# Kernel optimization log

Hardware: AMD Instinct MI355X
Metric: run time of the kernel (lower is better)

## Reference

```python
import jax, jax.numpy as jnp
import numpy as np

DIM = 192
HEADS = 4
CTX = 256
HID = int(DIM * 2.66)  # 510


def _dwconv(x, w):
    # x: (b,c,h,w), w: (c,1,3,3) depthwise
    return jax.lax.conv_general_dilated(
        x, w, window_strides=(1, 1), padding='SAME',
        dimension_numbers=('NCHW', 'OIHW', 'NCHW'),
        feature_group_count=x.shape[1])


def _conv1x1(x, w):
    # w: (out, in)
    return jnp.einsum('oc,bchw->bohw', w, x)


def _layernorm(x, weight, bias):
    # WithBias LayerNorm over channel dim (last dim after to_3d == channels)
    mu = x.mean(axis=1, keepdims=True)
    var = ((x - mu) ** 2).mean(axis=1, keepdims=True)
    xn = (x - mu) / jnp.sqrt(var + 1e-5)
    return xn * weight[None, :, None, None] + bias[None, :, None, None]


def setup_inputs() -> dict:
    key = jax.random.key(0)
    ks = jax.random.split(key, 16)
    s = 0.02
    inp = {
        'x': jax.random.normal(ks[0], (8, DIM, 128, 128), jnp.float32),
        'context_emb': jax.random.normal(ks[1], (8, CTX), jnp.float32),
        'ln1_w': jnp.ones((DIM,), jnp.float32),
        'ln1_b': jnp.zeros((DIM,), jnp.float32),
        'ln2_w': jnp.ones((DIM,), jnp.float32),
        'ln2_b': jnp.zeros((DIM,), jnp.float32),
        'w_qkv': jax.random.normal(ks[2], (3 * DIM, DIM), jnp.float32) * s,
        'w_qkv_dw': jax.random.normal(ks[3], (3 * DIM, 1, 3, 3), jnp.float32) * s,
        'w_proj': jax.random.normal(ks[4], (DIM, DIM), jnp.float32) * s,
        'base_temp': jnp.ones((HEADS, 1, 1), jnp.float32),
        'ta_w1': jax.random.normal(ks[5], (DIM // 4, CTX), jnp.float32) * s,
        'ta_b1': jnp.zeros((DIM // 4,), jnp.float32),
        'ta_w2': jax.random.normal(ks[6], (HEADS, DIM // 4), jnp.float32) * s,
        'ta_b2': jnp.zeros((HEADS,), jnp.float32),
        'vg_w': jax.random.normal(ks[7], (DIM, CTX), jnp.float32) * s,
        'vg_b': jnp.zeros((DIM,), jnp.float32),
        'w_local': jax.random.normal(ks[8], (DIM, 1, 3, 3), jnp.float32) * s,
        'w_ffn_in': jax.random.normal(ks[9], (2 * HID, DIM), jnp.float32) * s,
        'w_ffn_dw': jax.random.normal(ks[10], (2 * HID, 1, 3, 3), jnp.float32) * s,
        'w_ffn_out': jax.random.normal(ks[11], (DIM, HID), jnp.float32) * s,
    }
    return inp


def _forward(x, context_emb, ln1_w, ln1_b, ln2_w, ln2_b, w_qkv, w_qkv_dw,
             w_proj, base_temp, ta_w1, ta_b1, ta_w2, ta_b2, vg_w, vg_b,
             w_local, w_ffn_in, w_ffn_dw, w_ffn_out):
    b, c, h, w = x.shape
    hd = c // HEADS
    scale = hd ** (-0.5)

    # ---- Attention branch ----
    residual = x
    xn = _layernorm(x, ln1_w, ln1_b)

    # context adapters
    t = jax.nn.relu(context_emb @ ta_w1.T + ta_b1) @ ta_w2.T + ta_b2  # (b,heads)
    temp_factor = jax.nn.sigmoid(t)[:, :, None, None] * 2.0 + 0.5    # (b,heads,1,1)
    total_temp = base_temp[None] * temp_factor
    v_gate = jax.nn.sigmoid(context_emb @ vg_w.T + vg_b)             # (b,dim)
    v_gate = v_gate.reshape(b, HEADS, hd, 1)

    qkv = _dwconv(_conv1x1(xn, w_qkv), w_qkv_dw)
    q, k, v = jnp.split(qkv, 3, axis=1)

    def heads_flat(t4):
        return t4.reshape(b, HEADS, hd, h * w)

    qf = heads_flat(q)
    kf = heads_flat(k)
    vf = heads_flat(v)
    qf = qf / jnp.maximum(jnp.linalg.norm(qf, axis=-1, keepdims=True), 1e-12)
    kf = kf / jnp.maximum(jnp.linalg.norm(kf, axis=-1, keepdims=True), 1e-12)

    attn = jnp.einsum('bhcn,bhdn->bhcd', qf, kf) * scale  # (b,heads,hd,hd)
    attn = jax.nn.softmax(attn * total_temp, axis=-1)

    out_global = jnp.einsum('bhcd,bhdn->bhcn', attn, vf * v_gate)
    out_global = out_global.reshape(b, c, h, w)
    out_local = _dwconv(v, w_local)
    x = residual + _conv1x1(out_global + out_local, w_proj)

    # ---- GDFN branch ----
    residual = x
    xn = _layernorm(x, ln2_w, ln2_b)
    y = _dwconv(_conv1x1(xn, w_ffn_in), w_ffn_dw)
    y1, y2 = jnp.split(y, 2, axis=1)
    y = jax.nn.gelu(y1, approximate=False) * y2
    x = residual + _conv1x1(y, w_ffn_out)
    return x


def reference(x, context_emb, ln1_w, ln1_b, ln2_w, ln2_b, w_qkv, w_qkv_dw,
              w_proj, base_temp, ta_w1, ta_b1, ta_w2, ta_b2, vg_w, vg_b,
              w_local, w_ffn_in, w_ffn_dw, w_ffn_out):
    return _forward(x, context_emb, ln1_w, ln1_b, ln2_w, ln2_b, w_qkv,
                    w_qkv_dw, w_proj, base_temp, ta_w1, ta_b1, ta_w2, ta_b2,
                    vg_w, vg_b, w_local, w_ffn_in, w_ffn_dw, w_ffn_out)
```

## Files before the change

kernel.cpp:

```cpp
#include <hip/hip_runtime.h>
#include <math.h>

#define NB 8
#define NC 192
#define NH 128
#define NW 128
#define HW 16384
#define NQ 576
#define NHID 510
#define NHIDP 512
#define NG2 1020
#define NG2P 1024

#define BROWS 32
#define BSLOTS 34
#define BPIX (BSLOTS * NW)
#define BIPIX (BROWS * NW)

typedef unsigned short u16;
typedef short s16x8 __attribute__((ext_vector_type(8)));
typedef float f32x4 __attribute__((ext_vector_type(4)));

#define MFMA_BF16(a, b, c) __builtin_amdgcn_mfma_f32_16x16x32_bf16((a), (b), (c), 0, 0, 0)

__device__ __forceinline__ u16 f2bf(float f) {
  union { float f; unsigned u; } v; v.f = f;
  unsigned r = v.u + 0x7fffu + ((v.u >> 16) & 1u);
  return (u16)(r >> 16);
}
__device__ __forceinline__ float bf2f(u16 h) {
  union { unsigned u; float f; } v; v.u = ((unsigned)h) << 16; return v.f;
}
__device__ __forceinline__ float lo2f(unsigned u) {
  union { unsigned u; float f; } v; v.u = u << 16; return v.f;
}
__device__ __forceinline__ float hi2f(unsigned u) {
  union { unsigned u; float f; } v; v.u = u & 0xffff0000u; return v.f;
}

__global__ void k_prep(const float* __restrict__ wq, const float* __restrict__ wfi,
                       const float* __restrict__ wfo,
                       u16* __restrict__ oq, u16* __restrict__ ofi, u16* __restrict__ ofo) {
  const int n1 = NQ * NC, n2 = NG2P * NC, n3 = NC * NHIDP;
  for (int i = blockIdx.x * blockDim.x + threadIdx.x; i < n1 + n2 + n3;
       i += gridDim.x * blockDim.x) {
    if (i < n1) {
      oq[i] = f2bf(wq[i]);
    } else if (i < n1 + n2) {
      int j = i - n1; int row = j / NC;
      u16 v = 0;
      if (row < NG2) v = f2bf(wfi[j]);
      ofi[j] = v;
    } else {
      int j = i - n1 - n2; int row = j >> 9, col = j & 511;
      u16 v = 0;
      if (col < NHID) v = f2bf(wfo[row * NHID + col]);
      ofo[j] = v;
    }
  }
}

__global__ void k_ctx(const float* __restrict__ ce, const float* __restrict__ taw1,
                      const float* __restrict__ tab1, const float* __restrict__ taw2,
                      const float* __restrict__ tab2, const float* __restrict__ vgw,
                      const float* __restrict__ vgb, const float* __restrict__ btemp,
                      float* __restrict__ tempt, float* __restrict__ vg) {
  int b = blockIdx.x, t = threadIdx.x;
  __shared__ float sce[256];
  __shared__ float shid[48];
  sce[t] = ce[b * 256 + t];
  __syncthreads();
  if (t < 48) {
    float s = tab1[t];
    for (int j = 0; j < 256; j++) s = fmaf(taw1[t * 256 + j], sce[j], s);
    shid[t] = fmaxf(s, 0.f);
  }
  __syncthreads();
  if (t < 4) {
    float s = tab2[t];
    for (int j = 0; j < 48; j++) s = fmaf(taw2[t * 48 + j], shid[j], s);
    float sg = 1.f / (1.f + expf(-s));
    tempt[b * 4 + t] = btemp[t] * (sg * 2.f + 0.5f);
  }
  if (t < 192) {
    float s = vgb[t];
    for (int j = 0; j < 256; j++) s = fmaf(vgw[t * 256 + j], sce[j], s);
    vg[b * 192 + t] = 1.f / (1.f + expf(-s));
  }
}

__global__ __launch_bounds__(256, 2)
void k_ln_gemm_band(const float* __restrict__ in, const float* __restrict__ lnw,
                    const float* __restrict__ lnb, const u16* __restrict__ wbf,
                    u16* __restrict__ out, int nchunks, int row_start, int slot0) {
  __shared__ u16 Xn[64 * 200];
  __shared__ u16 Wc[64 * 200];
  __shared__ float red[512];
  __shared__ float stats[128];
  int t = threadIdx.x;
  int lane = t & 63, wv = t >> 6;
  int bpb = gridDim.x >> 3;
  int b = blockIdx.x / bpb;
  int rb = blockIdx.x - b * bpb;
  int gpx0 = row_start * NW + rb * 64;
  int opx0 = slot0 * NW + rb * 64;
  const float* xp = in + (size_t)b * NC * HW + gpx0 + lane;
  float vals[48];
  float s = 0.f, s2 = 0.f;
#pragma unroll
  for (int j = 0; j < 48; j++) {
    float v = xp[(size_t)(wv * 48 + j) * HW];
    vals[j] = v; s += v; s2 = fmaf(v, v, s2);
  }
  red[wv * 64 + lane] = s;
  red[256 + wv * 64 + lane] = s2;
  __syncthreads();
  if (t < 64) {
    float m = 0.f, q = 0.f;
#pragma unroll
    for (int k = 0; k < 4; k++) { m += red[k * 64 + t]; q += red[256 + k * 64 + t]; }
    m *= (1.f / 192.f);
    float var = q * (1.f / 192.f) - m * m;
    stats[t] = m; stats[64 + t] = rsqrtf(var + 1e-5f);
  }
  __syncthreads();
  float mu = stats[lane], rs = stats[64 + lane];
#pragma unroll
  for (int j = 0; j < 48; j += 2) {
    int c = wv * 48 + j;
    float xa = (vals[j] - mu) * rs * lnw[c] + lnb[c];
    float xb = (vals[j + 1] - mu) * rs * lnw[c + 1] + lnb[c + 1];
    *(unsigned*)&Xn[lane * 200 + c] = (unsigned)f2bf(xa) | ((unsigned)f2bf(xb) << 16);
  }
  int r = lane & 15, grp = lane >> 4;
  int ostride = nchunks << 6;
  for (int nc = 0; nc < nchunks; nc++) {
    __syncthreads();
    for (int i = t; i < 1536; i += 256) {
      int row = i / 24, sg = i % 24;
      *(s16x8*)&Wc[row * 200 + sg * 8] =
          *(const s16x8*)&wbf[(size_t)(nc * 64 + row) * 192 + sg * 8];
    }
    __syncthreads();
    f32x4 z = {0.f, 0.f, 0.f, 0.f};
    f32x4 acc0 = z, acc1 = z, acc2 = z, acc3 = z;
#pragma unroll
    for (int ks = 0; ks < 6; ks++) {
      int k0 = ks * 32 + grp * 8;
      s16x8 a = *(s16x8*)&Xn[(wv * 16 + r) * 200 + k0];
      acc0 = MFMA_BF16(a, *(s16x8*)&Wc[r * 200 + k0], acc0);
      acc1 = MFMA_BF16(a, *(s16x8*)&Wc[(16 + r) * 200 + k0], acc1);
      acc2 = MFMA_BF16(a, *(s16x8*)&Wc[(32 + r) * 200 + k0], acc2);
      acc3 = MFMA_BF16(a, *(s16x8*)&Wc[(48 + r) * 200 + k0], acc3);
    }
    u16* op = out + ((size_t)b * BPIX + opx0 + wv * 16 + grp * 4) * ostride + nc * 64 + r;
#pragma unroll
    for (int i = 0; i < 4; i++) {
      op[(size_t)i * ostride] = f2bf(acc0[i]);
      op[(size_t)i * ostride + 16] = f2bf(acc1[i]);
      op[(size_t)i * ostride + 32] = f2bf(acc2[i]);
      op[(size_t)i * ostride + 48] = f2bf(acc3[i]);
    }
  }
}

__global__ __launch_bounds__(256, 4)
void k_dw_attn_band(const u16* __restrict__ qb_band, const float* __restrict__ wdw,
                    u16* __restrict__ qkb, u16* __restrict__ vpm,
                    float* __restrict__ ssq, int r0) {
  __shared__ u16 Hl[6 * 18 * 64];
  __shared__ float sred[8 * 64];
  int t = threadIdx.x;
  int cc = blockIdx.x % 9;
  int rem = blockIdx.x / 9;
  int b = rem >> 6; int r2 = rem & 63;
  int h0l = (r2 >> 3) * 4, w0 = (r2 & 7) * 16;
  int c0 = cc * 64;
  const s16x8 z8 = {0, 0, 0, 0, 0, 0, 0, 0};
  for (int i = t; i < 864; i += 256) {
    int px = i >> 3, sg = i & 7;
    int hh = px / 18, ww = px % 18;
    int slot = h0l + hh;
    int gh = r0 - 1 + slot;
    int gw = w0 - 1 + ww;
    s16x8 v = z8;
    if (gh >= 0 && gh < NH && gw >= 0 && gw < NW)
      v = *(const s16x8*)&qb_band[((size_t)b * BPIX + slot * NW + gw) * NQ + c0 + sg * 8];
    *(s16x8*)&Hl[(hh * 18 + ww) * 64 + sg * 8] = v;
  }
  __syncthreads();
  int cp = t & 31, psub = t >> 5;
  int pr = psub >> 1, pc0 = (psub & 1) * 8;
  int gc = c0 + 2 * cp;
  float wg0[9], wg1[9];
#pragma unroll
  for (int q = 0; q < 9; q++) { wg0[q] = wdw[gc * 9 + q]; wg1[q] = wdw[(gc + 1) * 9 + q]; }
  bool isv = (c0 >= 384);
  float sq0 = 0.f, sq1 = 0.f;
  s16x8 ov0 = z8, ov1 = z8;
#pragma unroll
  for (int j = 0; j < 8; j++) {
    int pc = pc0 + j;
    float a0 = 0.f, a1 = 0.f;
#pragma unroll
    for (int dr = 0; dr < 3; dr++)
#pragma unroll
      for (int dc = 0; dc < 3; dc++) {
        unsigned u = *(const unsigned*)&Hl[((pr + dr) * 18 + pc + dc) * 64 + 2 * cp];
        a0 = fmaf(lo2f(u), wg0[dr * 3 + dc], a0);
        a1 = fmaf(hi2f(u), wg1[dr * 3 + dc], a1);
      }
    u16 u0 = f2bf(a0), u1 = f2bf(a1);
    if (isv) {
      int gp = (r0 + h0l + pr) * NW + w0 + pc;
      *(unsigned*)&vpm[((size_t)b * HW + gp) * 192 + (gc - 384)] =
          (unsigned)u0 | ((unsigned)u1 << 16);
    } else {
      ov0[j] = (short)u0; ov1[j] = (short)u1;
      float f0 = bf2f(u0), f1 = bf2f(u1);
      sq0 = fmaf(f0, f0, sq0); sq1 = fmaf(f1, f1, sq1);
    }
  }
  if (!isv) {
    int lpx = (h0l + pr) * NW + w0 + pc0;
    *(s16x8*)&qkb[((size_t)b * 384 + gc) * BIPIX + lpx] = ov0;
    *(s16x8*)&qkb[((size_t)b * 384 + gc + 1) * BIPIX + lpx] = ov1;
    sred[psub * 64 + 2 * cp] = sq0;
    sred[psub * 64 + 2 * cp + 1] = sq1;
    __syncthreads();
    if (t < 64) {
      float sa = 0.f;
#pragma unroll
      for (int p8 = 0; p8 < 8; p8++) sa += sred[p8 * 64 + t];
      atomicAdd(&ssq[b * 384 + c0 + t], sa);
    }
  }
}

__global__ __launch_bounds__(256, 2)
void k_attn_band(const u16* __restrict__ qkb, float* __restrict__ attn) {
  __shared__ float par[4 * 2304];
  int t = threadIdx.x;
  int lane = t & 63, wv = t >> 6;
  int r = lane & 15, grp = lane >> 4;
  int bh = blockIdx.x >> 2, kc = blockIdx.x & 3;
  int b = bh >> 2, h = bh & 3;
  const u16* qb = qkb + ((size_t)b * 384 + h * 48) * BIPIX;
  const u16* kb = qkb + ((size_t)b * 384 + 192 + h * 48) * BIPIX;
  f32x4 z = {0.f, 0.f, 0.f, 0.f};
  f32x4 acc[3][3];
#pragma unroll
  for (int i = 0; i < 3; i++)
#pragma unroll
    for (int j = 0; j < 3; j++) acc[i][j] = z;
  int kbase = kc * 1024 + wv * 256 + grp * 8;
#pragma unroll 2
  for (int ks = 0; ks < 8; ks++) {
    int k0 = kbase + ks * 32;
    s16x8 af[3], bf[3];
#pragma unroll
    for (int mt = 0; mt < 3; mt++) af[mt] = *(const s16x8*)&qb[(size_t)(mt * 16 + r) * BIPIX + k0];
#pragma unroll
    for (int nt = 0; nt < 3; nt++) bf[nt] = *(const s16x8*)&kb[(size_t)(nt * 16 + r) * BIPIX + k0];
#pragma unroll
    for (int mt = 0; mt < 3; mt++)
#pragma unroll
      for (int nt = 0; nt < 3; nt++) acc[mt][nt] = MFMA_BF16(af[mt], bf[nt], acc[mt][nt]);
  }
#pragma unroll
  for (int mt = 0; mt < 3; mt++)
#pragma unroll
    for (int nt = 0; nt < 3; nt++)
#pragma unroll
      for (int i = 0; i < 4; i++)
        par[wv * 2304 + (mt * 16 + grp * 4 + i) * 48 + nt * 16 + r] = acc[mt][nt][i];
  __syncthreads();
  float* ag = attn + (size_t)bh * 2304;
  for (int i = t; i < 2304; i += 256)
    atomicAdd(&ag[i], par[i] + par[2304 + i] + par[4608 + i] + par[6912 + i]);
}

__global__ void k_softmax(float* __restrict__ attn, const float* __restrict__ ssq,
                          const float* __restrict__ tempt, const float* __restrict__ vg) {
  int bh = blockIdx.x, b = bh >> 2, h = bh & 3;
  int t = threadIdx.x;
  __shared__ float srk[48], svg[48];
  if (t < 48) {
    float nk = sqrtf(ssq[b * 384 + 192 + h * 48 + t]);
    srk[t] = 1.f / fmaxf(nk, 1e-12f);
    svg[t] = vg[b * 192 + h * 48 + t];
  }
  __syncthreads();
  if (t < 48) {
    float nq = sqrtf(ssq[b * 384 + h * 48 + t]);
    float rq = 1.f / fmaxf(nq, 1e-12f);
    float sc = 0.14433756729740643f * tempt[b * 4 + h] * rq;
    float* row = attn + (size_t)bh * 2304 + t * 48;
    float l[48]; float mx = -1e30f;
#pragma unroll
    for (int d = 0; d < 48; d++) { l[d] = row[d] * srk[d] * sc; mx = fmaxf(mx, l[d]); }
    float ss = 0.f;
#pragma unroll
    for (int d = 0; d < 48; d++) { l[d] = expf(l[d] - mx); ss += l[d]; }
    float inv = 1.f / ss;
#pragma unroll
    for (int d = 0; d < 48; d++) row[d] = l[d] * inv * svg[d];
  }
}

__global__ __launch_bounds__(256)
void k_wd(const float* __restrict__ attn, const float* __restrict__ wp,
          u16* __restrict__ wdg) {
  __shared__ float am[4 * 48 * 48];
  int b = blockIdx.x >> 3, oc = blockIdx.x & 7;
  int t = threadIdx.x;
  const float* ag = attn + (size_t)b * 4 * 2304;
  for (int i = t; i < 9216; i += 256) am[i] = ag[i];
  __syncthreads();
  u16* wdb = wdg + (size_t)b * 192 * 384;
  for (int idx = t; idx < 24 * 384; idx += 256) {
    int oo = idx / 384, j = idx % 384;
    int o = oc * 24 + oo;
    float val;
    if (j < 192) {
      int hj = j / 48, dj = j % 48;
      const float* wpo = wp + o * 192 + hj * 48;
      const float* ap = am + hj * 2304 + dj;
      float sa = 0.f;
#pragma unroll
      for (int c = 0; c < 48; c++) sa = fmaf(wpo[c], ap[c * 48], sa);
      val = sa;
    } else {
      val = wp[o * 192 + (j - 192)];
    }
    wdb[o * 384 + j] = f2bf(val);
  }
}

__global__ __launch_bounds__(256, 2)
void k_proj(const u16* __restrict__ vpm, const float* __restrict__ wl,
            const u16* __restrict__ wdg, const float* __restrict__ x,
            float* __restrict__ x2) {
  __shared__ u16 Hl[6 * 18 * 64];
  __shared__ u16 Xl[64 * 392];
  int t = threadIdx.x;
  int b = blockIdx.x >> 8; int r2 = blockIdx.x & 255;
  int h0 = (r2 >> 3) * 4, w0 = (r2 & 7) * 16;
  int cp = t & 31, psub = t >> 5;
  int pr = psub >> 1, pc0 = (psub & 1) * 8;
  int lane = t & 63, wv = t >> 6;
  int r = lane & 15, grp = lane >> 4;
  float xres[3][4][4];
#pragma unroll
  for (int mt = 0; mt < 3; mt++)
#pragma unroll
    for (int nt = 0; nt < 4; nt++) {
      size_t base = ((size_t)b * NC + wv * 48 + mt * 16 + grp * 4) * HW +
                    (h0 + nt) * NW + w0 + r;
#pragma unroll
      for (int i = 0; i < 4; i++) xres[mt][nt][i] = x[base + (size_t)i * HW];
    }
  const s16x8 z8 = {0, 0, 0, 0, 0, 0, 0, 0};
  for (int c3 = 0; c3 < 3; c3++) {
    int c0 = c3 * 64;
    __syncthreads();
    for (int i = t; i < 864; i += 256) {
      int px = i >> 3, sg = i & 7;
      int hh = px / 18, ww = px % 18;
      int gh = h0 - 1 + hh, gw = w0 - 1 + ww;
      s16x8 v = z8;
      if (gh >= 0 && gh < NH && gw >= 0 && gw < NW)
        v = *(const s16x8*)&vpm[((size_t)b * HW + gh * NW + gw) * 192 + c0 + sg * 8];
      *(s16x8*)&Hl[(hh * 18 + ww) * 64 + sg * 8] = v;
    }
    __syncthreads();
    int gc = c0 + 2 * cp;
    float wg0[9], wg1[9];
#pragma unroll
    for (int q = 0; q < 9; q++) { wg0[q] = wl[gc * 9 + q]; wg1[q] = wl[(gc + 1) * 9 + q]; }
#pragma unroll
    for (int j = 0; j < 8; j++) {
      int pc = pc0 + j; int p = pr * 16 + pc;
      float a0 = 0.f, a1 = 0.f; unsigned uc = 0;
#pragma unroll
      for (int dr = 0; dr < 3; dr++)
#pragma unroll
        for (int dc = 0; dc < 3; dc++) {
          unsigned u = *(const unsigned*)&Hl[((pr + dr) * 18 + pc + dc) * 64 + 2 * cp];
          if (dr == 1 && dc == 1) uc = u;
          a0 = fmaf(lo2f(u), wg0[dr * 3 + dc], a0);
          a1 = fmaf(hi2f(u), wg1[dr * 3 + dc], a1);
        }
      *(unsigned*)&Xl[p * 392 + gc] = uc;
      *(unsigned*)&Xl[p * 392 + 192 + gc] =
          (unsigned)f2bf(a0) | ((unsigned)f2bf(a1) << 16);
    }
  }
  __syncthreads();
  const u16* wdb = wdg + (size_t)b * 192 * 384;
  f32x4 z = {0.f, 0.f, 0.f, 0.f};
  f32x4 acc[3][4];
#pragma unroll
  for (int i = 0; i < 3; i++)
#pragma unroll
    for (int j = 0; j < 4; j++) acc[i][j] = z;
#pragma unroll 2
  for (int ks = 0; ks < 12; ks++) {
    int k0 = ks * 32 + grp * 8;
    s16x8 b0 = *(s16x8*)&Xl[r * 392 + k0];
    s16x8 b1 = *(s16x8*)&Xl[(16 + r) * 392 + k0];
    s16x8 b2 = *(s16x8*)&Xl[(32 + r) * 392 + k0];
    s16x8 b3 = *(s16x8*)&Xl[(48 + r) * 392 + k0];
#pragma unroll
    for (int mt = 0; mt < 3; mt++) {
      s16x8 a = *(const s16x8*)&wdb[(size_t)(wv * 48 + mt * 16 + r) * 384 + k0];
      acc[mt][0] = MFMA_BF16(a, b0, acc[mt][0]);
      acc[mt][1] = MFMA_BF16(a, b1, acc[mt][1]);
      acc[mt][2] = MFMA_BF16(a, b2, acc[mt][2]);
      acc[mt][3] = MFMA_BF16(a, b3, acc[mt][3]);
    }
  }
#pragma unroll
  for (int mt = 0; mt < 3; mt++)
#pragma unroll
    for (int nt = 0; nt < 4; nt++) {
      size_t base = ((size_t)b * NC + wv * 48 + mt * 16 + grp * 4) * HW +
                    (h0 + nt) * NW + w0 + r;
#pragma unroll
      for (int i = 0; i < 4; i++) {
        size_t idx = base + (size_t)i * HW;
        x2[idx] = acc[mt][nt][i] + xres[mt][nt][i];
      }
    }
}

__global__ __launch_bounds__(256, 2)
void k_gelu_ffn_band(const u16* __restrict__ ypre, const float* __restrict__ wdwf,
                     const u16* __restrict__ wfo, const float* __restrict__ x2,
                     float* __restrict__ out, int r0) {
  __shared__ u16 H1[6 * 18 * 64];
  __shared__ u16 H2[6 * 18 * 72];
  __shared__ u16 Yc[64 * 80];
  int t = threadIdx.x;
  int b = blockIdx.x >> 6; int r2 = blockIdx.x & 63;
  int h0l = (r2 >> 3) * 4, w0 = (r2 & 7) * 16;
  int cp = t & 31, psub = t >> 5;
  int pr = psub >> 1, pc0 = (psub & 1) * 8;
  int lane = t & 63, wv = t >> 6;
  int r = lane & 15, grp = lane >> 4;
  int jl = 2 * cp;
  float x2res[3][4][4];
#pragma unroll
  for (int mt = 0; mt < 3; mt++)
#pragma unroll
    for (int nt = 0; nt < 4; nt++) {
      size_t base = ((size_t)b * NC + wv * 48 + mt * 16 + grp * 4) * HW +
                    (r0 + h0l + nt) * NW + w0 + r;
#pragma unroll
      for (int i = 0; i < 4; i++) x2res[mt][nt][i] = x2[base + (size_t)i * HW];
    }
  const s16x8 z8 = {0, 0, 0, 0, 0, 0, 0, 0};
  f32x4 z = {0.f, 0.f, 0.f, 0.f};
  f32x4 acc[3][4];
#pragma unroll
  for (int i = 0; i < 3; i++)
#pragma unroll
    for (int j = 0; j < 4; j++) acc[i][j] = z;

  for (int jc = 0; jc < 8; jc++) {
    int j0 = jc * 64;
    int base2 = j0 + 504;
    __syncthreads();
    for (int i = t; i < 864; i += 256) {
      int px = i >> 3, sg = i & 7;
      int hh = px / 18, ww = px % 18;
      int slot = h0l + hh;
      int gh = r0 - 1 + slot, gw = w0 - 1 + ww;
      s16x8 v = z8;
      if (gh >= 0 && gh < NH && gw >= 0 && gw < NW)
        v = *(const s16x8*)&ypre[((size_t)b * BPIX + slot * NW + gw) * NG2P + j0 + sg * 8];
      *(s16x8*)&H1[(hh * 18 + ww) * 64 + sg * 8] = v;
    }
    for (int i = t; i < 972; i += 256) {
      int px = i / 9, sg = i % 9;
      int hh = px / 18, ww = px % 18;
      int slot = h0l + hh;
      int gh = r0 - 1 + slot, gw = w0 - 1 + ww;
      s16x8 v = z8;
      if (gh >= 0 && gh < NH && gw >= 0 && gw < NW)
        v = *(const s16x8*)&ypre[((size_t)b * BPIX + slot * NW + gw) * NG2P + base2 + sg * 8];
      *(s16x8*)&H2[(hh * 18 + ww) * 72 + sg * 8] = v;
    }
    __syncthreads();
    int j = j0 + jl;
    bool v0 = (j < NHID), v1 = (j + 1 < NHID);
    float w1a[9], w1b[9], w2a[9], w2b[9];
#pragma unroll
    for (int q = 0; q < 9; q++) {
      w1a[q] = 0.f; w1b[q] = 0.f; w2a[q] = 0.f; w2b[q] = 0.f;
      if (v0) { w1a[q] = wdwf[j * 9 + q]; w2a[q] = wdwf[(j + NHID) * 9 + q]; }
      if (v1) { w1b[q] = wdwf[(j + 1) * 9 + q]; w2b[q] = wdwf[(j + 1 + NHID) * 9 + q]; }
    }
#pragma unroll
    for (int jj = 0; jj < 8; jj++) {
      int pc = pc0 + jj;
      float d1a = 0.f, d1b = 0.f, d2a = 0.f, d2b = 0.f;
#pragma unroll
      for (int dr = 0; dr < 3; dr++)
#pragma unroll
        for (int dc = 0; dc < 3; dc++) {
          int q = dr * 3 + dc;
          unsigned u1 = *(const unsigned*)&H1[((pr + dr) * 18 + pc + dc) * 64 + jl];
          unsigned u2 = *(const unsigned*)&H2[((pr + dr) * 18 + pc + dc) * 72 + jl + 6];
          d1a = fmaf(lo2f(u1), w1a[q], d1a); d1b = fmaf(hi2f(u1), w1b[q], d1b);
          d2a = fmaf(lo2f(u2), w2a[q], d2a); d2b = fmaf(hi2f(u2), w2b[q], d2b);
        }
      float ga = 0.5f * d1a * (1.f + erff(d1a * 0.70710678118654752f));
      float gb = 0.5f * d1b * (1.f + erff(d1b * 0.70710678118654752f));
      float ya = v0 ? ga * d2a : 0.f;
      float yb = v1 ? gb * d2b : 0.f;
      int lp = pr * 16 + pc;
      *(unsigned*)&Yc[lp * 80 + jl] = (unsigned)f2bf(ya) | ((unsigned)f2bf(yb) << 16);
    }
    __syncthreads();
#pragma unroll
    for (int ks = 0; ks < 2; ks++) {
      int k0 = ks * 32 + grp * 8;
      s16x8 b0 = *(s16x8*)&Yc[r * 80 + k0];
      s16x8 b1 = *(s16x8*)&Yc[(16 + r) * 80 + k0];
      s16x8 b2 = *(s16x8*)&Yc[(32 + r) * 80 + k0];
      s16x8 b3 = *(s16x8*)&Yc[(48 + r) * 80 + k0];
#pragma unroll
      for (int mt = 0; mt < 3; mt++) {
        s16x8 a = *(const s16x8*)&wfo[(size_t)(wv * 48 + mt * 16 + r) * NHIDP + j0 + k0];
        acc[mt][0] = MFMA_BF16(a, b0, acc[mt][0]);
        acc[mt][1] = MFMA_BF16(a, b1, acc[mt][1]);
        acc[mt][2] = MFMA_BF16(a, b2, acc[mt][2]);
        acc[mt][3] = MFMA_BF16(a, b3, acc[mt][3]);
      }
    }
  }
#pragma unroll
  for (int mt = 0; mt < 3; mt++)
#pragma unroll
    for (int nt = 0; nt < 4; nt++) {
      size_t base = ((size_t)b * NC + wv * 48 + mt * 16 + grp * 4) * HW +
                    (r0 + h0l + nt) * NW + w0 + r;
#pragma unroll
      for (int i = 0; i < 4; i++) {
        size_t idx = base + (size_t)i * HW;
        out[idx] = acc[mt][nt][i] + x2res[mt][nt][i];
      }
    }
}

extern "C" void kernel_launch(void* const* d_in, const int* in_sizes, int n_in,
                              void* d_out, int out_size, void* d_ws, size_t ws_size,
                              hipStream_t stream) {
  const float* x      = (const float*)d_in[0];
  const float* ce     = (const float*)d_in[1];
  const float* ln1w   = (const float*)d_in[2];
  const float* ln1b   = (const float*)d_in[3];
  const float* ln2w   = (const float*)d_in[4];
  const float* ln2b   = (const float*)d_in[5];
  const float* wqkv   = (const float*)d_in[6];
  const float* wqkvdw = (const float*)d_in[7];
  const float* wproj  = (const float*)d_in[8];
  const float* btemp  = (const float*)d_in[9];
  const float* taw1   = (const float*)d_in[10];
  const float* tab1   = (const float*)d_in[11];
  const float* taw2   = (const float*)d_in[12];
  const float* tab2   = (const float*)d_in[13];
  const float* vgw    = (const float*)d_in[14];
  const float* vgb    = (const float*)d_in[15];
  const float* wlocal = (const float*)d_in[16];
  const float* wffni  = (const float*)d_in[17];
  const float* wffndw = (const float*)d_in[18];
  const float* wffno  = (const float*)d_in[19];
  float* outp = (float*)d_out;
  char* ws = (char*)d_ws;

  const size_t REQUIRED = 224602240ULL;
  if (ws_size < REQUIRED) {
    hipMemsetAsync(d_out, 0, (size_t)out_size * 4, stream);
    return;
  }
  u16*   wq_bf   = (u16*)(ws + 0);
  u16*   wfi_bf  = (u16*)(ws + 221184);
  u16*   wfo_bf  = (u16*)(ws + 614400);
  float* tempt   = (float*)(ws + 811008);
  float* vg      = (float*)(ws + 811136);
  float* ssq     = (float*)(ws + 817280);
  float* attn    = (float*)(ws + 829568);
  u16*   wdg     = (u16*)(ws + 1124480);
  u16*   qkvband = (u16*)(ws + 2304128);
  u16*   qkband  = (u16*)(ws + 42412160);
  u16*   ypreband= (u16*)(ws + 2304128);
  u16*   vpm     = (u16*)(ws + 73607296);
  float* x2      = (float*)(ws + 123938944);

  hipMemsetAsync(ws + 817280, 0, 12288 + 294912, stream);
  k_prep<<<512, 256, 0, stream>>>(wqkv, wffni, wffno, wq_bf, wfi_bf, wfo_bf);
  k_ctx<<<8, 256, 0, stream>>>(ce, taw1, tab1, taw2, tab2, vgw, vgb, btemp, tempt, vg);

  for (int band = 0; band < 4; band++) {
    int r0 = band * BROWS;
    int rs = (r0 > 0) ? r0 - 1 : 0;
    int re = (r0 + BROWS + 1 < NH) ? r0 + BROWS + 1 : NH;
    int nr = re - rs;
    int s0 = rs - (r0 - 1);
    k_ln_gemm_band<<<8 * nr * 2, 256, 0, stream>>>(x, ln1w, ln1b, wq_bf, qkvband, 9, rs, s0);
    k_dw_attn_band<<<9 * 8 * 64, 256, 0, stream>>>(qkvband, wqkvdw, qkband, vpm, ssq, r0);
    k_attn_band<<<32 * 4, 256, 0, stream>>>(qkband, attn);
  }
  k_softmax<<<32, 64, 0, stream>>>(attn, ssq, tempt, vg);
  k_wd<<<64, 256, 0, stream>>>(attn, wproj, wdg);
  k_proj<<<2048, 256, 0, stream>>>(vpm, wlocal, wdg, x, x2);

  for (int band = 0; band < 4; band++) {
    int r0 = band * BROWS;
    int rs = (r0 > 0) ? r0 - 1 : 0;
    int re = (r0 + BROWS + 1 < NH) ? r0 + BROWS + 1 : NH;
    int nr = re - rs;
    int s0 = rs - (r0 - 1);
    k_ln_gemm_band<<<8 * nr * 2, 256, 0, stream>>>(x2, ln2w, ln2b, wfi_bf, ypreband, 16, rs, s0);
    k_gelu_ffn_band<<<8 * 64, 256, 0, stream>>>(ypreband, wffndw, wfo_bf, x2, outp, r0);
  }
}
```

Before: 1.268 ms.

## Double-buffer halo tiles via direct global-to-LDS loads in depthwise kernels

Halo tile staging in the depthwise-conv kernels now uses direct global-to-LDS 16-byte loads, with out-of-bounds pixels pointing at a zeroed scratch buffer instead of taking a register path. k_proj and k_gelu_ffn_band double-buffer these tiles so the next channel chunk is fetched while the current one is computed, removing one barrier per iteration. The FFN kernel also stops holding residual values in registers and reads them at the epilogue, to ease register pressure. Doubling the LDS buffers may reduce occupancy.

Result: faster. 1.114 ms (-12.2%).

```diff
diff --git a/kernel.cpp b/kernel.cpp
--- a/kernel.cpp
+++ b/kernel.cpp
@@ -36,6 +36,12 @@
 }
 __device__ __forceinline__ float hi2f(unsigned u) {
   union { unsigned u; float f; } v; v.u = u & 0xffff0000u; return v.f;
+}
+
+__device__ __forceinline__ void gll16(const void* g, void* l) {
+  __builtin_amdgcn_global_load_lds(
+      (const __attribute__((address_space(1))) void*)g,
+      (__attribute__((address_space(3))) void*)l, 16, 0, 0);
 }
 
 __global__ void k_prep(const float* __restrict__ wq, const float* __restrict__ wfi,
@@ -167,7 +173,7 @@
 __global__ __launch_bounds__(256, 4)
 void k_dw_attn_band(const u16* __restrict__ qb_band, const float* __restrict__ wdw,
                     u16* __restrict__ qkb, u16* __restrict__ vpm,
-                    float* __restrict__ ssq, int r0) {
+                    float* __restrict__ ssq, int r0, const u16* __restrict__ zp) {
   __shared__ u16 Hl[6 * 18 * 64];
   __shared__ float sred[8 * 64];
   int t = threadIdx.x;
@@ -183,10 +189,10 @@
     int slot = h0l + hh;
     int gh = r0 - 1 + slot;
     int gw = w0 - 1 + ww;
-    s16x8 v = z8;
-    if (gh >= 0 && gh < NH && gw >= 0 && gw < NW)
-      v = *(const s16x8*)&qb_band[((size_t)b * BPIX + slot * NW + gw) * NQ + c0 + sg * 8];
-    *(s16x8*)&Hl[(hh * 18 + ww) * 64 + sg * 8] = v;
+    const void* g = (gh >= 0 && gh < NH && gw >= 0 && gw < NW)
+        ? (const void*)&qb_band[((size_t)b * BPIX + slot * NW + gw) * NQ + c0 + sg * 8]
+        : (const void*)zp;
+    gll16(g, &Hl[i * 8]);
   }
   __syncthreads();
   int cp = t & 31, psub = t >> 5;
@@ -340,8 +346,8 @@
 __global__ __launch_bounds__(256, 2)
 void k_proj(const u16* __restrict__ vpm, const float* __restrict__ wl,
             const u16* __restrict__ wdg, const float* __restrict__ x,
-            float* __restrict__ x2) {
-  __shared__ u16 Hl[6 * 18 * 64];
+            float* __restrict__ x2, const u16* __restrict__ zp) {
+  __shared__ u16 Hl[2][6 * 18 * 64];
   __shared__ u16 Xl[64 * 392];
   int t = threadIdx.x;
   int b = blockIdx.x >> 8; int r2 = blockIdx.x & 255;
@@ -360,20 +366,26 @@
 #pragma unroll
       for (int i = 0; i < 4; i++) xres[mt][nt][i] = x[base + (size_t)i * HW];
     }
-  const s16x8 z8 = {0, 0, 0, 0, 0, 0, 0, 0};
-  for (int c3 = 0; c3 < 3; c3++) {
-    int c0 = c3 * 64;
-    __syncthreads();
+
+  auto stageH = [&](int c3s, int buf) {
+    int c0s = c3s * 64;
     for (int i = t; i < 864; i += 256) {
       int px = i >> 3, sg = i & 7;
       int hh = px / 18, ww = px % 18;
       int gh = h0 - 1 + hh, gw = w0 - 1 + ww;
-      s16x8 v = z8;
-      if (gh >= 0 && gh < NH && gw >= 0 && gw < NW)
-        v = *(const s16x8*)&vpm[((size_t)b * HW + gh * NW + gw) * 192 + c0 + sg * 8];
-      *(s16x8*)&Hl[(hh * 18 + ww) * 64 + sg * 8] = v;
-    }
-    __syncthreads();
+      const void* g = (gh >= 0 && gh < NH && gw >= 0 && gw < NW)
+          ? (const void*)&vpm[((size_t)b * HW + gh * NW + gw) * 192 + c0s + sg * 8]
+          : (const void*)zp;
+      gll16(g, &Hl[buf][i * 8]);
+    }
+  };
+
+  stageH(0, 0);
+  __syncthreads();
+  int cur = 0;
+  for (int c3 = 0; c3 < 3; c3++) {
+    if (c3 < 2) stageH(c3 + 1, cur ^ 1);
+    int c0 = c3 * 64;
     int gc = c0 + 2 * cp;
     float wg0[9], wg1[9];
 #pragma unroll
@@ -386,7 +398,7 @@
       for (int dr = 0; dr < 3; dr++)
 #pragma unroll
         for (int dc = 0; dc < 3; dc++) {
-          unsigned u = *(const unsigned*)&Hl[((pr + dr) * 18 + pc + dc) * 64 + 2 * cp];
+          unsigned u = *(const unsigned*)&Hl[cur][((pr + dr) * 18 + pc + dc) * 64 + 2 * cp];
           if (dr == 1 && dc == 1) uc = u;
           a0 = fmaf(lo2f(u), wg0[dr * 3 + dc], a0);
           a1 = fmaf(hi2f(u), wg1[dr * 3 + dc], a1);
@@ -395,8 +407,9 @@
       *(unsigned*)&Xl[p * 392 + 192 + gc] =
           (unsigned)f2bf(a0) | ((unsigned)f2bf(a1) << 16);
     }
-  }
-  __syncthreads();
+    __syncthreads();
+    cur ^= 1;
+  }
   const u16* wdb = wdg + (size_t)b * 192 * 384;
   f32x4 z = {0.f, 0.f, 0.f, 0.f};
   f32x4 acc[3][4];
@@ -437,9 +450,9 @@
 __global__ __launch_bounds__(256, 2)
 void k_gelu_ffn_band(const u16* __restrict__ ypre, const float* __restrict__ wdwf,
                      const u16* __restrict__ wfo, const float* __restrict__ x2,
-                     float* __restrict__ out, int r0) {
-  __shared__ u16 H1[6 * 18 * 64];
-  __shared__ u16 H2[6 * 18 * 72];
+                     float* __restrict__ out, int r0, const u16* __restrict__ zp) {
+  __shared__ u16 H1[2][6 * 18 * 64];
+  __shared__ u16 H2[2][6 * 18 * 72];
   __shared__ u16 Yc[64 * 80];
   int t = threadIdx.x;
   int b = blockIdx.x >> 6; int r2 = blockIdx.x & 63;
@@ -449,49 +462,45 @@
   int lane = t & 63, wv = t >> 6;
   int r = lane & 15, grp = lane >> 4;
   int jl = 2 * cp;
-  float x2res[3][4][4];
-#pragma unroll
-  for (int mt = 0; mt < 3; mt++)
-#pragma unroll
-    for (int nt = 0; nt < 4; nt++) {
-      size_t base = ((size_t)b * NC + wv * 48 + mt * 16 + grp * 4) * HW +
-                    (r0 + h0l + nt) * NW + w0 + r;
-#pragma unroll
-      for (int i = 0; i < 4; i++) x2res[mt][nt][i] = x2[base + (size_t)i * HW];
-    }
-  const s16x8 z8 = {0, 0, 0, 0, 0, 0, 0, 0};
-  f32x4 z = {0.f, 0.f, 0.f, 0.f};
-  f32x4 acc[3][4];
-#pragma unroll
-  for (int i = 0; i < 3; i++)
-#pragma unroll
-    for (int j = 0; j < 4; j++) acc[i][j] = z;
-
-  for (int jc = 0; jc < 8; jc++) {
-    int j0 = jc * 64;
-    int base2 = j0 + 504;
-    __syncthreads();
+
+  auto stage = [&](int jc, int buf) {
+    int j0s = jc * 64;
+    int base2 = j0s + 504;
     for (int i = t; i < 864; i += 256) {
       int px = i >> 3, sg = i & 7;
       int hh = px / 18, ww = px % 18;
       int slot = h0l + hh;
       int gh = r0 - 1 + slot, gw = w0 - 1 + ww;
-      s16x8 v = z8;
-      if (gh >= 0 && gh < NH && gw >= 0 && gw < NW)
-        v = *(const s16x8*)&ypre[((size_t)b * BPIX + slot * NW + gw) * NG2P + j0 + sg * 8];
-      *(s16x8*)&H1[(hh * 18 + ww) * 64 + sg * 8] = v;
+      const void* g = (gh >= 0 && gh < NH && gw >= 0 && gw < NW)
+          ? (const void*)&ypre[((size_t)b * BPIX + slot * NW + gw) * NG2P + j0s + sg * 8]
+          : (const void*)zp;
+      gll16(g, &H1[buf][i * 8]);
     }
     for (int i = t; i < 972; i += 256) {
-      int px = i / 9, sg = i % 9;
+      int px = i / 9, sg = i - px * 9;
       int hh = px / 18, ww = px % 18;
       int slot = h0l + hh;
       int gh = r0 - 1 + slot, gw = w0 - 1 + ww;
-      s16x8 v = z8;
-      if (gh >= 0 && gh < NH && gw >= 0 && gw < NW)
-        v = *(const s16x8*)&ypre[((size_t)b * BPIX + slot * NW + gw) * NG2P + base2 + sg * 8];
-      *(s16x8*)&H2[(hh * 18 + ww) * 72 + sg * 8] = v;
-    }
-    __syncthreads();
+      const void* g = (gh >= 0 && gh < NH && gw >= 0 && gw < NW)
+          ? (const void*)&ypre[((size_t)b * BPIX + slot * NW + gw) * NG2P + base2 + sg * 8]
+          : (const void*)zp;
+      gll16(g, &H2[buf][i * 8]);
+    }
+  };
+
+  f32x4 z = {0.f, 0.f, 0.f, 0.f};
+  f32x4 acc[3][4];
+#pragma unroll
+  for (int i = 0; i < 3; i++)
+#pragma unroll
+    for (int j = 0; j < 4; j++) acc[i][j] = z;
+
+  stage(0, 0);
+  __syncthreads();
+  int cur = 0;
+  for (int jc = 0; jc < 8; jc++) {
+    if (jc < 7) stage(jc + 1, cur ^ 1);
+    int j0 = jc * 64;
     int j = j0 + jl;
     bool v0 = (j < NHID), v1 = (j + 1 < NHID);
     float w1a[9], w1b[9], w2a[9], w2b[9];
@@ -510,8 +519,8 @@
 #pragma unroll
         for (int dc = 0; dc < 3; dc++) {
           int q = dr * 3 + dc;
-          unsigned u1 = *(const unsigned*)&H1[((pr + dr) * 18 + pc + dc) * 64 + jl];
-          unsigned u2 = *(const unsigned*)&H2[((pr + dr) * 18 + pc + dc) * 72 + jl + 6];
+          unsigned u1 = *(const unsigned*)&H1[cur][((pr + dr) * 18 + pc + dc) * 64 + jl];
+          unsigned u2 = *(const unsigned*)&H2[cur][((pr + dr) * 18 + pc + dc) * 72 + jl + 6];
           d1a = fmaf(lo2f(u1), w1a[q], d1a); d1b = fmaf(hi2f(u1), w1b[q], d1b);
           d2a = fmaf(lo2f(u2), w2a[q], d2a); d2b = fmaf(hi2f(u2), w2b[q], d2b);
         }
@@ -539,6 +548,8 @@
         acc[mt][3] = MFMA_BF16(a, b3, acc[mt][3]);
       }
     }
+    __syncthreads();
+    cur ^= 1;
   }
 #pragma unroll
   for (int mt = 0; mt < 3; mt++)
@@ -549,7 +560,7 @@
 #pragma unroll
       for (int i = 0; i < 4; i++) {
         size_t idx = base + (size_t)i * HW;
-        out[idx] = acc[mt][nt][i] + x2res[mt][nt][i];
+        out[idx] = acc[mt][nt][i] + x2[idx];
       }
     }
 }
@@ -580,7 +591,7 @@
   float* outp = (float*)d_out;
   char* ws = (char*)d_ws;
 
-  const size_t REQUIRED = 224602240ULL;
+  const size_t REQUIRED = 224602496ULL;
   if (ws_size < REQUIRED) {
     hipMemsetAsync(d_out, 0, (size_t)out_size * 4, stream);
     return;
@@ -598,8 +609,10 @@
   u16*   ypreband= (u16*)(ws + 2304128);
   u16*   vpm     = (u16*)(ws + 73607296);
   float* x2      = (float*)(ws + 123938944);
+  u16*   zp      = (u16*)(ws + 224602240);
 
   hipMemsetAsync(ws + 817280, 0, 12288 + 294912, stream);
+  hipMemsetAsync(ws + 224602240, 0, 256, stream);
   k_prep<<<512, 256, 0, stream>>>(wqkv, wffni, wffno, wq_bf, wfi_bf, wfo_bf);
   k_ctx<<<8, 256, 0, stream>>>(ce, taw1, tab1, taw2, tab2, vgw, vgb, btemp, tempt, vg);
 
@@ -610,12 +623,12 @@
     int nr = re - rs;
     int s0 = rs - (r0 - 1);
     k_ln_gemm_band<<<8 * nr * 2, 256, 0, stream>>>(x, ln1w, ln1b, wq_bf, qkvband, 9, rs, s0);
-    k_dw_attn_band<<<9 * 8 * 64, 256, 0, stream>>>(qkvband, wqkvdw, qkband, vpm, ssq, r0);
+    k_dw_attn_band<<<9 * 8 * 64, 256, 0, stream>>>(qkvband, wqkvdw, qkband, vpm, ssq, r0, zp);
     k_attn_band<<<32 * 4, 256, 0, stream>>>(qkband, attn);
   }
   k_softmax<<<32, 64, 0, stream>>>(attn, ssq, tempt, vg);
   k_wd<<<64, 256, 0, stream>>>(attn, wproj, wdg);
-  k_proj<<<2048, 256, 0, stream>>>(vpm, wlocal, wdg, x, x2);
+  k_proj<<<2048, 256, 0, stream>>>(vpm, wlocal, wdg, x, x2, zp);
 
   for (int band = 0; band < 4; band++) {
     int r0 = band * BROWS;
@@ -624,6 +637,6 @@
     int nr = re - rs;
     int s0 = rs - (r0 - 1);
     k_ln_gemm_band<<<8 * nr * 2, 256, 0, stream>>>(x2, ln2w, ln2b, wfi_bf, ypreband, 16, rs, s0);
-    k_gelu_ffn_band<<<8 * 64, 256, 0, stream>>>(ypreband, wffndw, wfo_bf, x2, outp, r0);
-  }
-}
+    k_gelu_ffn_band<<<8 * 64, 256, 0, stream>>>(ypreband, wffndw, wfo_bf, x2, outp, r0, zp);
+  }
+}
```
